# Kernel tuning notes

Measured on AMD Instinct MI355X. Metric: run time of the kernel, lower is better.

The kernel has to match this reference:

```python
import jax, jax.numpy as jnp
import numpy as np

N = 50000
E = 800000
IN = 3
H = 64
OUT = 128
L = 4


def _layernorm(x, w, b, eps=1e-5):
    mu = jnp.mean(x, axis=-1, keepdims=True)
    var = jnp.mean(jnp.square(x - mu), axis=-1, keepdims=True)
    return (x - mu) * jax.lax.rsqrt(var + eps) * w + b


def setup_inputs() -> dict:
    key = jax.random.key(0)
    ks = jax.random.split(key, 12)

    def lin(k, fan_in, shape):
        return jax.random.normal(k, shape, dtype=jnp.float32) / np.sqrt(fan_in)

    x = jax.random.normal(ks[0], (N, IN), dtype=jnp.float32)
    edge_index = jax.random.randint(ks[1], (2, E), 0, N, dtype=jnp.int32)
    return {
        "x": x,
        "edge_index": edge_index,
        "in_w": lin(ks[2], IN, (IN, H)), "in_b": jnp.zeros((H,), jnp.float32),
        "ew1": lin(ks[3], 2, (2, H)), "eb1": jnp.zeros((H,), jnp.float32),
        "ew2": lin(ks[4], H, (H, H)), "eb2": jnp.zeros((H,), jnp.float32),
        "cw1": lin(ks[5], H, (L, H, H)), "cb1": jnp.zeros((L, H), jnp.float32),
        "cw2": lin(ks[6], H, (L, H, H)), "cb2": jnp.zeros((L, H), jnp.float32),
        "lnw": jnp.ones((L, H), jnp.float32), "lnb": jnp.zeros((L, H), jnp.float32),
        "fw": lin(ks[7], H, (H, OUT)), "fb": jnp.zeros((OUT,), jnp.float32),
        "rw": lin(ks[8], H, (H, OUT)), "rb": jnp.zeros((OUT,), jnp.float32),
        "ow": jnp.ones((OUT,), jnp.float32), "ob": jnp.zeros((OUT,), jnp.float32),
    }


def reference(x, edge_index, in_w, in_b, ew1, eb1, ew2, eb2,
              cw1, cb1, cw2, cb2, lnw, lnb, fw, fb, rw, rb, ow, ob):
    pos = x[:, :2]
    row, col = edge_index[0], edge_index[1]  # source, target (PyG convention)
    rel_pos = pos[col] - pos[row]                              # [E, 2]
    edge_attr = jnp.maximum(rel_pos @ ew1 + eb1, 0.0) @ ew2 + eb2  # [E, H]

    h = x @ in_w + in_b  # [N, H]
    for i in range(L):
        identity = h
        # GINEConv (eps=0): mlp(x_i + sum_j relu(x_j + e_ij))
        msg = jax.nn.relu(h[row] + edge_attr)                  # [E, H]
        agg = jax.ops.segment_sum(msg, col, num_segments=N)    # [N, H]
        m = h + agg
        m = jnp.maximum(m @ cw1[i] + cb1[i], 0.0) @ cw2[i] + cb2[i]
        m = _layernorm(m, lnw[i], lnb[i])
        h = jax.nn.gelu(m, approximate=False) + identity

    out = (h @ fw + fb) + (h @ rw + rb)
    return _layernorm(out, ow, ob)
```

## Files before the change

### kernel.cpp

```cpp
#include <hip/hip_runtime.h>
#include <hip/hip_fp16.h>
#include <stdint.h>

#define NN 50000
#define NE 800000
#define SCAN_BLOCKS 196

typedef _Float16 half8v __attribute__((ext_vector_type(8)));
typedef float f32x4 __attribute__((ext_vector_type(4)));

static __device__ __forceinline__ __half2 u2h2(unsigned int u) {
    union { unsigned int u; __half2 h; } c; c.u = u; return c.h;
}
static __device__ __forceinline__ unsigned int h22u(__half2 h) {
    union { __half2 h; unsigned int u; } c; c.h = h; return c.u;
}

static __device__ __forceinline__ float4 fma4(float4 a, float s, float4 w) {
    a.x = fmaf(s, w.x, a.x); a.y = fmaf(s, w.y, a.y);
    a.z = fmaf(s, w.z, a.z); a.w = fmaf(s, w.w, a.w);
    return a;
}
static __device__ __forceinline__ void acch(float4& acc, uint2 h, uint2 e) {
    float2 h0 = __half22float2(u2h2(h.x));
    float2 h1 = __half22float2(u2h2(h.y));
    float2 e0 = __half22float2(u2h2(e.x));
    float2 e1 = __half22float2(u2h2(e.y));
    acc.x += fmaxf(h0.x + e0.x, 0.f);
    acc.y += fmaxf(h0.y + e0.y, 0.f);
    acc.z += fmaxf(h1.x + e1.x, 0.f);
    acc.w += fmaxf(h1.y + e1.y, 0.f);
}

__global__ __launch_bounds__(256) void k_deg(const int* __restrict__ ei, int* __restrict__ offcur) {
    int e = blockIdx.x * 256 + threadIdx.x;
    atomicAdd(&offcur[ei[NE + e]], 1);
}

__global__ __launch_bounds__(256) void k_scanA(const int* __restrict__ off, int* __restrict__ part) {
    __shared__ int s[256];
    int t = threadIdx.x;
    int idx = blockIdx.x * 256 + t;
    int d = (idx < NN) ? off[idx] : 0;
    s[t] = d; __syncthreads();
    for (int o = 128; o > 0; o >>= 1) {
        if (t < o) s[t] += s[t + o];
        __syncthreads();
    }
    if (t == 0) part[blockIdx.x] = s[0];
}

__global__ __launch_bounds__(256) void k_scanB(int* __restrict__ part) {
    __shared__ int s[256];
    int t = threadIdx.x;
    int d = (t < SCAN_BLOCKS) ? part[t] : 0;
    s[t] = d; __syncthreads();
    #pragma unroll
    for (int o = 1; o < 256; o <<= 1) {
        int v = (t >= o) ? s[t - o] : 0;
        __syncthreads();
        s[t] += v;
        __syncthreads();
    }
    if (t < SCAN_BLOCKS) part[t] = s[t] - d;
}

__global__ __launch_bounds__(256) void k_scanC(int* __restrict__ off, const int* __restrict__ part) {
    __shared__ int s[256];
    int t = threadIdx.x;
    int idx = blockIdx.x * 256 + t;
    int d = (idx < NN) ? off[idx] : 0;
    s[t] = d; __syncthreads();
    #pragma unroll
    for (int o = 1; o < 256; o <<= 1) {
        int v = (t >= o) ? s[t - o] : 0;
        __syncthreads();
        s[t] += v;
        __syncthreads();
    }
    if (idx < NN) off[idx] = s[t] - d + part[blockIdx.x];
}

__global__ __launch_bounds__(256) void k_scatter(const int* __restrict__ ei,
        int* __restrict__ offcur, unsigned short* __restrict__ rows, int* __restrict__ dpos) {
    int e = blockIdx.x * 256 + threadIdx.x;
    int col = ei[NE + e];
    int pos = atomicAdd(&offcur[col], 1);
    rows[pos] = (unsigned short)ei[e];
    dpos[e] = pos;
}

__global__ __launch_bounds__(256) void k_prep(const float* __restrict__ ew2, __half* __restrict__ w2f) {
    int tid = threadIdx.x;
    for (int i = tid; i < 4096; i += 256) {
        int k = i >> 6, n = i & 63;
        int kt = k >> 5, kin = k & 31;
        int quad = kin >> 3, j = kin & 7;
        int nt = n >> 4, nin = n & 15;
        w2f[(size_t)((kt * 4 + nt) * 64 + quad * 16 + nin) * 8 + j] = __float2half(ew2[i]);
    }
}

__global__ __launch_bounds__(256) void k_input(const float* __restrict__ x,
        const float* __restrict__ in_w, const float* __restrict__ in_b,
        __half* __restrict__ Ah) {
    int n = blockIdx.x * 4 + (threadIdx.x >> 6);
    int k = threadIdx.x & 63;
    const float* xr = x + (size_t)n * 3;
    float v = in_b[k] + xr[0] * in_w[k] + xr[1] * in_w[64 + k] + xr[2] * in_w[128 + k];
    Ah[(size_t)n * 64 + k] = __float2half(v);
}

__global__ __launch_bounds__(256) void k_edge(const float* __restrict__ x,
        const int* __restrict__ ei,
        const float* __restrict__ ew1, const float* __restrict__ eb1,
        const float* __restrict__ eb2, const __half* __restrict__ w2f,
        const int* __restrict__ dpos, __half* __restrict__ ea) {
    __shared__ float s_w1[128], s_b1[64], s_b2[64];
    __shared__ float s_rx[256], s_ry[256];
    __shared__ int s_pos[256];
    __shared__ __half s_d[4][16][80];
    int tid = threadIdx.x, lane = tid & 63, w = tid >> 6;

    half8v bf[8];
    {
        const half8v* W2F = (const half8v*)w2f;
        #pragma unroll
        for (int f = 0; f < 8; ++f) bf[f] = W2F[f * 64 + lane];
    }
    if (tid < 128) s_w1[tid] = ew1[tid];
    if (tid < 64) s_b1[tid] = eb1[tid];
    else if (tid < 128) s_b2[tid - 64] = eb2[tid - 64];
    int eb = blockIdx.x * 256;
    {
        int e = eb + tid;
        int r = ei[e], c = ei[NE + e];
        s_rx[tid] = x[(size_t)c * 3]     - x[(size_t)r * 3];
        s_ry[tid] = x[(size_t)c * 3 + 1] - x[(size_t)r * 3 + 1];
        s_pos[tid] = dpos[e];
    }
    __syncthreads();

    int lm = lane & 15, lq = lane >> 4;
    #pragma unroll
    for (int t = 0; t < 4; ++t) {
        int ebase = w * 64 + t * 16;
        float rx = s_rx[ebase + lm], ry = s_ry[ebase + lm];
        half8v a0, a1;
        #pragma unroll
        for (int j = 0; j < 8; ++j) {
            int k0 = lq * 8 + j;
            a0[j] = (_Float16)fmaxf(fmaf(rx, s_w1[k0], fmaf(ry, s_w1[64 + k0], s_b1[k0])), 0.f);
            int k1 = k0 + 32;
            a1[j] = (_Float16)fmaxf(fmaf(rx, s_w1[k1], fmaf(ry, s_w1[64 + k1], s_b1[k1])), 0.f);
        }
        f32x4 acc[4];
        #pragma unroll
        for (int nt = 0; nt < 4; ++nt) {
            float b = s_b2[nt * 16 + lm];
            acc[nt][0] = b; acc[nt][1] = b; acc[nt][2] = b; acc[nt][3] = b;
            acc[nt] = __builtin_amdgcn_mfma_f32_16x16x32_f16(a0, bf[nt],     acc[nt], 0, 0, 0);
            acc[nt] = __builtin_amdgcn_mfma_f32_16x16x32_f16(a1, bf[4 + nt], acc[nt], 0, 0, 0);
        }
        __builtin_amdgcn_wave_barrier();
        #pragma unroll
        for (int nt = 0; nt < 4; ++nt)
            #pragma unroll
            for (int r = 0; r < 4; ++r)
                s_d[w][lq * 4 + r][nt * 16 + lm] = __float2half(acc[nt][r]);
        __builtin_amdgcn_wave_barrier();
        int row = lane >> 2, seg = lane & 3;
        int pos = s_pos[w * 64 + t * 16 + row];
        uint4 v0 = *(const uint4*)&s_d[w][row][seg * 16];
        uint4 v1 = *(const uint4*)&s_d[w][row][seg * 16 + 8];
        uint4* dst = (uint4*)&ea[(size_t)pos * 64 + seg * 16];
        dst[0] = v0;
        dst[1] = v1;
        __builtin_amdgcn_wave_barrier();
    }
}

__global__ __launch_bounds__(256) void k_agg(const __half* __restrict__ Ah,
        const __half* __restrict__ ea, const unsigned short* __restrict__ rows,
        const int* __restrict__ offcur, float* __restrict__ M) {
    const uint2* A2 = (const uint2*)Ah;
    const uint2* E2 = (const uint2*)ea;
    int w = threadIdx.x >> 6, lane = threadIdx.x & 63;
    int es = lane >> 4, ch = lane & 15;
    int n = blockIdx.x * 4 + w;
    int p0 = (n == 0) ? 0 : offcur[n - 1];
    int p1 = offcur[n];
    float4 acc = {0,0,0,0}, accB = {0,0,0,0};
    for (int base = p0; base < p1; base += 64) {
        int cnt = min(64, p1 - base);
        int rl = (int)rows[base + min(lane, cnt - 1)];
        int j = 0;
        for (; j + 8 <= cnt; j += 8) {
            int i0 = j + es, i1 = j + 4 + es;
            int r0 = __shfl(rl, i0, 64);
            int r1 = __shfl(rl, i1, 64);
            uint2 h0 = A2[(size_t)r0 * 16 + ch];
            uint2 h1 = A2[(size_t)r1 * 16 + ch];
            uint2 e0 = E2[(size_t)(base + i0) * 16 + ch];
            uint2 e1 = E2[(size_t)(base + i1) * 16 + ch];
            acch(acc, h0, e0);
            acch(accB, h1, e1);
        }
        for (; j < cnt; j += 4) {
            int i0 = j + es;
            bool valid = i0 < cnt;
            int ic = valid ? i0 : (cnt - 1);
            int r0 = __shfl(rl, ic, 64);
            uint2 h0 = A2[(size_t)r0 * 16 + ch];
            uint2 e0 = E2[(size_t)(base + ic) * 16 + ch];
            if (valid) acch(acc, h0, e0);
        }
    }
    acc.x += accB.x; acc.y += accB.y; acc.z += accB.z; acc.w += accB.w;
    #pragma unroll
    for (int m = 16; m < 64; m <<= 1) {
        acc.x += __shfl_xor(acc.x, m, 64);
        acc.y += __shfl_xor(acc.y, m, 64);
        acc.z += __shfl_xor(acc.z, m, 64);
        acc.w += __shfl_xor(acc.w, m, 64);
    }
    if (es == 0) {
        uint2 su = A2[(size_t)n * 16 + ch];
        float2 s0 = __half22float2(u2h2(su.x));
        float2 s1 = __half22float2(u2h2(su.y));
        float4 o;
        o.x = s0.x + acc.x; o.y = s0.y + acc.y;
        o.z = s1.x + acc.z; o.w = s1.y + acc.w;
        *(float4*)&M[(size_t)n * 64 + ch * 4] = o;
    }
}

__global__ __launch_bounds__(256) void k_node(__half* __restrict__ Ah, const float* __restrict__ M,
        const float* __restrict__ cw1, const float* __restrict__ cb1,
        const float* __restrict__ cw2, const float* __restrict__ cb2,
        const float* __restrict__ lnw, const float* __restrict__ lnb) {
    __shared__ float s_W1[64 * 64];
    __shared__ float s_W2[64 * 64];
    __shared__ float s_m[64 * 68];
    __shared__ float s_b1[64], s_b2[64], s_g[64], s_bt[64];
    int tid = threadIdx.x;
    for (int i = tid; i < 4096; i += 256) { s_W1[i] = cw1[i]; s_W2[i] = cw2[i]; }
    if (tid < 64) { s_b1[tid] = cb1[tid]; s_g[tid] = lnw[tid]; }
    else if (tid < 128) { s_b2[tid - 64] = cb2[tid - 64]; s_bt[tid - 64] = lnb[tid - 64]; }
    int nb = blockIdx.x * 64;
    {
        const float4* M4 = (const float4*)(M + (size_t)nb * 64);
        #pragma unroll
        for (int q = 0; q < 4; ++q) {
            int i = q * 1024 + tid * 4;
            int nl = i >> 6, k = i & 63;
            float4 v = {0,0,0,0};
            if (nb + nl < NN) v = M4[i >> 2];
            *(float4*)&s_m[nl * 68 + k] = v;
        }
    }
    __syncthreads();

    int lane = tid & 63, w = tid >> 6;
    int cq = lane & 15, ng = lane >> 4;
    int rbase = w * 16 + ng * 4;
    int c0 = cq * 4;

    float4 acc[4];
    {
        float4 b1q = *(const float4*)&s_b1[c0];
        acc[0] = b1q; acc[1] = b1q; acc[2] = b1q; acc[3] = b1q;
    }
    #pragma unroll 4
    for (int k4 = 0; k4 < 16; ++k4) {
        float4 m0 = *(const float4*)&s_m[(rbase + 0) * 68 + k4 * 4];
        float4 m1 = *(const float4*)&s_m[(rbase + 1) * 68 + k4 * 4];
        float4 m2 = *(const float4*)&s_m[(rbase + 2) * 68 + k4 * 4];
        float4 m3 = *(const float4*)&s_m[(rbase + 3) * 68 + k4 * 4];
        #pragma unroll
        for (int kk = 0; kk < 4; ++kk) {
            float4 w4 = *(const float4*)&s_W1[(k4 * 4 + kk) * 64 + c0];
            acc[0] = fma4(acc[0], ((const float*)&m0)[kk], w4);
            acc[1] = fma4(acc[1], ((const float*)&m1)[kk], w4);
            acc[2] = fma4(acc[2], ((const float*)&m2)[kk], w4);
            acc[3] = fma4(acc[3], ((const float*)&m3)[kk], w4);
        }
    }
    __builtin_amdgcn_wave_barrier();
    #pragma unroll
    for (int j = 0; j < 4; ++j) {
        float4 u;
        u.x = fmaxf(acc[j].x, 0.f); u.y = fmaxf(acc[j].y, 0.f);
        u.z = fmaxf(acc[j].z, 0.f); u.w = fmaxf(acc[j].w, 0.f);
        *(float4*)&s_m[(rbase + j) * 68 + c0] = u;
    }
    __builtin_amdgcn_wave_barrier();

    {
        float4 b2q = *(const float4*)&s_b2[c0];
        acc[0] = b2q; acc[1] = b2q; acc[2] = b2q; acc[3] = b2q;
    }
    #pragma unroll 4
    for (int k4 = 0; k4 < 16; ++k4) {
        float4 m0 = *(const float4*)&s_m[(rbase + 0) * 68 + k4 * 4];
        float4 m1 = *(const float4*)&s_m[(rbase + 1) * 68 + k4 * 4];
        float4 m2 = *(const float4*)&s_m[(rbase + 2) * 68 + k4 * 4];
        float4 m3 = *(const float4*)&s_m[(rbase + 3) * 68 + k4 * 4];
        #pragma unroll
        for (int kk = 0; kk < 4; ++kk) {
            float4 w4 = *(const float4*)&s_W2[(k4 * 4 + kk) * 64 + c0];
            acc[0] = fma4(acc[0], ((const float*)&m0)[kk], w4);
            acc[1] = fma4(acc[1], ((const float*)&m1)[kk], w4);
            acc[2] = fma4(acc[2], ((const float*)&m2)[kk], w4);
            acc[3] = fma4(acc[3], ((const float*)&m3)[kk], w4);
        }
    }

    float4 gq  = *(const float4*)&s_g[c0];
    float4 btq = *(const float4*)&s_bt[c0];
    #pragma unroll
    for (int j = 0; j < 4; ++j) {
        float4 v = acc[j];
        float sum = v.x + v.y + v.z + v.w;
        float sq  = v.x * v.x + v.y * v.y + v.z * v.z + v.w * v.w;
        #pragma unroll
        for (int m = 1; m < 16; m <<= 1) {
            sum += __shfl_xor(sum, m, 64);
            sq  += __shfl_xor(sq, m, 64);
        }
        float mu  = sum * (1.f / 64.f);
        float var = sq * (1.f / 64.f) - mu * mu;
        float rs  = rsqrtf(var + 1e-5f);
        int n = nb + rbase + j;
        if (n < NN) {
            uint2 iu = *(const uint2*)&Ah[(size_t)n * 64 + c0];
            float2 i0 = __half22float2(u2h2(iu.x));
            float2 i1 = __half22float2(u2h2(iu.y));
            float4 o;
            float y;
            y = (v.x - mu) * rs * gq.x + btq.x; o.x = 0.5f * y * (1.f + erff(y * 0.70710678118654752f)) + i0.x;
            y = (v.y - mu) * rs * gq.y + btq.y; o.y = 0.5f * y * (1.f + erff(y * 0.70710678118654752f)) + i0.y;
            y = (v.z - mu) * rs * gq.z + btq.z; o.z = 0.5f * y * (1.f + erff(y * 0.70710678118654752f)) + i1.x;
            y = (v.w - mu) * rs * gq.w + btq.w; o.w = 0.5f * y * (1.f + erff(y * 0.70710678118654752f)) + i1.y;
            uint2 ou;
            ou.x = h22u(__floats2half2_rn(o.x, o.y));
            ou.y = h22u(__floats2half2_rn(o.z, o.w));
            *(uint2*)&Ah[(size_t)n * 64 + c0] = ou;
        }
    }
}

__global__ __launch_bounds__(256) void k_final(const __half* __restrict__ Ah,
        const float* __restrict__ fw, const float* __restrict__ fb,
        const float* __restrict__ rw, const float* __restrict__ rb,
        const float* __restrict__ ow, const float* __restrict__ ob,
        float* __restrict__ out) {
    __shared__ float s_W[64 * 128];
    __shared__ float s_h[32 * 68];
    __shared__ float s_b[128];
    __shared__ float s_red[32][4];
    int tid = threadIdx.x;
    for (int i = tid; i < 8192; i += 256) s_W[i] = fw[i] + rw[i];
    if (tid < 128) s_b[tid] = fb[tid] + rb[tid];
    int nb = blockIdx.x * 32;
    for (int i = tid; i < 2048; i += 256) {
        int nl = i >> 6, k = i & 63;
        int n = nb + nl;
        s_h[nl * 68 + k] = (n < NN) ? __half2float(Ah[(size_t)n * 64 + k]) : 0.f;
    }
    __syncthreads();

    int lane = tid & 63, w = tid >> 6;
    int chh = w & 1, nh = w >> 1;
    int cq = lane & 15, ng = lane >> 4;
    int c0 = chh * 64 + cq * 4;
    int rbase = nh * 16 + ng * 4;

    float4 acc[4];
    {
        float4 bq = *(const float4*)&s_b[c0];
        acc[0] = bq; acc[1] = bq; acc[2] = bq; acc[3] = bq;
    }
    #pragma unroll 4
    for (int k4 = 0; k4 < 16; ++k4) {
        float4 m0 = *(const float4*)&s_h[(rbase + 0) * 68 + k4 * 4];
        float4 m1 = *(const float4*)&s_h[(rbase + 1) * 68 + k4 * 4];
        float4 m2 = *(const float4*)&s_h[(rbase + 2) * 68 + k4 * 4];
        float4 m3 = *(const float4*)&s_h[(rbase + 3) * 68 + k4 * 4];
        #pragma unroll
        for (int kk = 0; kk < 4; ++kk) {
            float4 w4 = *(const float4*)&s_W[(k4 * 4 + kk) * 128 + c0];
            acc[0] = fma4(acc[0], ((const float*)&m0)[kk], w4);
            acc[1] = fma4(acc[1], ((const float*)&m1)[kk], w4);
            acc[2] = fma4(acc[2], ((const float*)&m2)[kk], w4);
            acc[3] = fma4(acc[3], ((const float*)&m3)[kk], w4);
        }
    }
    #pragma unroll
    for (int j = 0; j < 4; ++j) {
        float4 v = acc[j];
        float sum = v.x + v.y + v.z + v.w;
        float sq  = v.x * v.x + v.y * v.y + v.z * v.z + v.w * v.w;
        #pragma unroll
        for (int m = 1; m < 16; m <<= 1) {
            sum += __shfl_xor(sum, m, 64);
            sq  += __shfl_xor(sq, m, 64);
        }
        if (cq == 0) {
            s_red[rbase + j][chh * 2]     = sum;
            s_red[rbase + j][chh * 2 + 1] = sq;
        }
    }
    __syncthreads();
    float4 gq = *(const float4*)&ow[c0];
    float4 bq = *(const float4*)&ob[c0];
    #pragma unroll
    for (int j = 0; j < 4; ++j) {
        int nl = rbase + j;
        int n = nb + nl;
        float tsum = s_red[nl][0] + s_red[nl][2];
        float tsq  = s_red[nl][1] + s_red[nl][3];
        float mu  = tsum * (1.f / 128.f);
        float var = tsq * (1.f / 128.f) - mu * mu;
        float rs  = rsqrtf(var + 1e-5f);
        if (n < NN) {
            float4 v = acc[j];
            float4 o;
            o.x = (v.x - mu) * rs * gq.x + bq.x;
            o.y = (v.y - mu) * rs * gq.y + bq.y;
            o.z = (v.z - mu) * rs * gq.z + bq.z;
            o.w = (v.w - mu) * rs * gq.w + bq.w;
            *(float4*)&out[(size_t)n * 128 + c0] = o;
        }
    }
}

extern "C" void kernel_launch(void* const* d_in, const int* in_sizes, int n_in,
                              void* d_out, int out_size, void* d_ws, size_t ws_size,
                              hipStream_t stream) {
    const float* x    = (const float*)d_in[0];
    const int*   ei   = (const int*)d_in[1];
    const float* in_w = (const float*)d_in[2];
    const float* in_b = (const float*)d_in[3];
    const float* ew1  = (const float*)d_in[4];
    const float* eb1  = (const float*)d_in[5];
    const float* ew2  = (const float*)d_in[6];
    const float* eb2  = (const float*)d_in[7];
    const float* cw1  = (const float*)d_in[8];
    const float* cb1  = (const float*)d_in[9];
    const float* cw2  = (const float*)d_in[10];
    const float* cb2  = (const float*)d_in[11];
    const float* lnw  = (const float*)d_in[12];
    const float* lnb  = (const float*)d_in[13];
    const float* fw   = (const float*)d_in[14];
    const float* fb   = (const float*)d_in[15];
    const float* rw   = (const float*)d_in[16];
    const float* rb   = (const float*)d_in[17];
    const float* ow   = (const float*)d_in[18];
    const float* ob   = (const float*)d_in[19];
    float* out = (float*)d_out;

    char* ws = (char*)d_ws;
    __half*         ea   = (__half*)ws;
    __half*         Ah   = (__half*)(ws + 102400000);
    unsigned short* rows = (unsigned short*)(ws + 108800000);
    int*            off  = (int*)(ws + 110400000);
    float*          M    = (float*)(ws + 110600016);
    int*            dpos = (int*)M;
    int*            part = (int*)((char*)M + 3200000);
    __half*         w2f  = (__half*)((char*)M + 3300000);

    (void)hipMemsetAsync(off, 0, (NN + 1) * sizeof(int), stream);
    k_deg<<<NE / 256, 256, 0, stream>>>(ei, off);
    k_scanA<<<SCAN_BLOCKS, 256, 0, stream>>>(off, part);
    k_scanB<<<1, 256, 0, stream>>>(part);
    k_scanC<<<SCAN_BLOCKS, 256, 0, stream>>>(off, part);
    k_scatter<<<NE / 256, 256, 0, stream>>>(ei, off, rows, dpos);
    k_prep<<<1, 256, 0, stream>>>(ew2, w2f);
    k_input<<<NN / 4, 256, 0, stream>>>(x, in_w, in_b, Ah);
    k_edge<<<NE / 256, 256, 0, stream>>>(x, ei, ew1, eb1, eb2, w2f, dpos, ea);

    const int nodeBlocks = (NN + 63) / 64;
    for (int l = 0; l < 4; ++l) {
        k_agg<<<NN / 4, 256, 0, stream>>>(Ah, ea, rows, off, M);
        k_node<<<nodeBlocks, 256, 0, stream>>>(Ah, M,
            cw1 + (size_t)l * 4096, cb1 + (size_t)l * 64,
            cw2 + (size_t)l * 4096, cb2 + (size_t)l * 64,
            lnw + (size_t)l * 64,   lnb + (size_t)l * 64);
    }
    k_final<<<(NN + 31) / 32, 256, 0, stream>>>(Ah, fw, fb, rw, rb, ow, ob, out);
}
```

Measured before the change: 507.8 us.

## Fuse CSR scatter into edge kernel, widen agg loads, store M as fp16

Removes the separate k_scatter kernel by doing the atomic slot allocation and row write inside k_edge, which also drops the dpos buffer round trip. k_agg now loads 16-byte vectors (8 halfs per lane, 8 lanes per row) and handles 16 edges per iteration instead of 8. The aggregated M buffer is stored in fp16 rather than fp32, halving its write and read traffic between k_agg and k_node. The cost is an extra rounding of h+agg to half precision and atomics moved into the edge kernel.

```diff
diff --git a/kernel.cpp b/kernel.cpp
--- a/kernel.cpp
+++ b/kernel.cpp
@@ -21,15 +21,16 @@
     a.z = fmaf(s, w.z, a.z); a.w = fmaf(s, w.w, a.w);
     return a;
 }
-static __device__ __forceinline__ void acch(float4& acc, uint2 h, uint2 e) {
-    float2 h0 = __half22float2(u2h2(h.x));
-    float2 h1 = __half22float2(u2h2(h.y));
-    float2 e0 = __half22float2(u2h2(e.x));
-    float2 e1 = __half22float2(u2h2(e.y));
-    acc.x += fmaxf(h0.x + e0.x, 0.f);
-    acc.y += fmaxf(h0.y + e0.y, 0.f);
-    acc.z += fmaxf(h1.x + e1.x, 0.f);
-    acc.w += fmaxf(h1.y + e1.y, 0.f);
+static __device__ __forceinline__ void acc8(float* acc, float4 hv, float4 ev) {
+    const unsigned int* hu = (const unsigned int*)&hv;
+    const unsigned int* eu = (const unsigned int*)&ev;
+    #pragma unroll
+    for (int q = 0; q < 4; ++q) {
+        float2 hf = __half22float2(u2h2(hu[q]));
+        float2 ef = __half22float2(u2h2(eu[q]));
+        acc[q * 2]     += fmaxf(hf.x + ef.x, 0.f);
+        acc[q * 2 + 1] += fmaxf(hf.y + ef.y, 0.f);
+    }
 }
 
 __global__ __launch_bounds__(256) void k_deg(const int* __restrict__ ei, int* __restrict__ offcur) {
@@ -81,15 +82,6 @@
     if (idx < NN) off[idx] = s[t] - d + part[blockIdx.x];
 }
 
-__global__ __launch_bounds__(256) void k_scatter(const int* __restrict__ ei,
-        int* __restrict__ offcur, unsigned short* __restrict__ rows, int* __restrict__ dpos) {
-    int e = blockIdx.x * 256 + threadIdx.x;
-    int col = ei[NE + e];
-    int pos = atomicAdd(&offcur[col], 1);
-    rows[pos] = (unsigned short)ei[e];
-    dpos[e] = pos;
-}
-
 __global__ __launch_bounds__(256) void k_prep(const float* __restrict__ ew2, __half* __restrict__ w2f) {
     int tid = threadIdx.x;
     for (int i = tid; i < 4096; i += 256) {
@@ -115,7 +107,8 @@
         const int* __restrict__ ei,
         const float* __restrict__ ew1, const float* __restrict__ eb1,
         const float* __restrict__ eb2, const __half* __restrict__ w2f,
-        const int* __restrict__ dpos, __half* __restrict__ ea) {
+        int* __restrict__ offcur, unsigned short* __restrict__ rows,
+        __half* __restrict__ ea) {
     __shared__ float s_w1[128], s_b1[64], s_b2[64];
     __shared__ float s_rx[256], s_ry[256];
     __shared__ int s_pos[256];
@@ -137,7 +130,9 @@
         int r = ei[e], c = ei[NE + e];
         s_rx[tid] = x[(size_t)c * 3]     - x[(size_t)r * 3];
         s_ry[tid] = x[(size_t)c * 3 + 1] - x[(size_t)r * 3 + 1];
-        s_pos[tid] = dpos[e];
+        int pos = atomicAdd(&offcur[c], 1);
+        rows[pos] = (unsigned short)r;
+        s_pos[tid] = pos;
     }
     __syncthreads();
 
@@ -182,60 +177,62 @@
 
 __global__ __launch_bounds__(256) void k_agg(const __half* __restrict__ Ah,
         const __half* __restrict__ ea, const unsigned short* __restrict__ rows,
-        const int* __restrict__ offcur, float* __restrict__ M) {
-    const uint2* A2 = (const uint2*)Ah;
-    const uint2* E2 = (const uint2*)ea;
+        const int* __restrict__ offcur, __half* __restrict__ M) {
+    const float4* A4 = (const float4*)Ah;
+    const float4* E4 = (const float4*)ea;
     int w = threadIdx.x >> 6, lane = threadIdx.x & 63;
-    int es = lane >> 4, ch = lane & 15;
+    int es = lane >> 3, oc = lane & 7;
     int n = blockIdx.x * 4 + w;
     int p0 = (n == 0) ? 0 : offcur[n - 1];
     int p1 = offcur[n];
-    float4 acc = {0,0,0,0}, accB = {0,0,0,0};
+    float acc[8] = {0,0,0,0,0,0,0,0};
+    float accB[8] = {0,0,0,0,0,0,0,0};
     for (int base = p0; base < p1; base += 64) {
         int cnt = min(64, p1 - base);
         int rl = (int)rows[base + min(lane, cnt - 1)];
         int j = 0;
-        for (; j + 8 <= cnt; j += 8) {
-            int i0 = j + es, i1 = j + 4 + es;
+        for (; j + 16 <= cnt; j += 16) {
+            int i0 = j + es, i1 = j + 8 + es;
             int r0 = __shfl(rl, i0, 64);
             int r1 = __shfl(rl, i1, 64);
-            uint2 h0 = A2[(size_t)r0 * 16 + ch];
-            uint2 h1 = A2[(size_t)r1 * 16 + ch];
-            uint2 e0 = E2[(size_t)(base + i0) * 16 + ch];
-            uint2 e1 = E2[(size_t)(base + i1) * 16 + ch];
-            acch(acc, h0, e0);
-            acch(accB, h1, e1);
-        }
-        for (; j < cnt; j += 4) {
+            float4 h0 = A4[(size_t)r0 * 8 + oc];
+            float4 h1 = A4[(size_t)r1 * 8 + oc];
+            float4 e0 = E4[(size_t)(base + i0) * 8 + oc];
+            float4 e1 = E4[(size_t)(base + i1) * 8 + oc];
+            acc8(acc, h0, e0);
+            acc8(accB, h1, e1);
+        }
+        for (; j < cnt; j += 8) {
             int i0 = j + es;
             bool valid = i0 < cnt;
             int ic = valid ? i0 : (cnt - 1);
             int r0 = __shfl(rl, ic, 64);
-            uint2 h0 = A2[(size_t)r0 * 16 + ch];
-            uint2 e0 = E2[(size_t)(base + ic) * 16 + ch];
-            if (valid) acch(acc, h0, e0);
-        }
-    }
-    acc.x += accB.x; acc.y += accB.y; acc.z += accB.z; acc.w += accB.w;
-    #pragma unroll
-    for (int m = 16; m < 64; m <<= 1) {
-        acc.x += __shfl_xor(acc.x, m, 64);
-        acc.y += __shfl_xor(acc.y, m, 64);
-        acc.z += __shfl_xor(acc.z, m, 64);
-        acc.w += __shfl_xor(acc.w, m, 64);
+            float4 h0 = A4[(size_t)r0 * 8 + oc];
+            float4 e0 = E4[(size_t)(base + ic) * 8 + oc];
+            if (valid) acc8(acc, h0, e0);
+        }
+    }
+    #pragma unroll
+    for (int q = 0; q < 8; ++q) acc[q] += accB[q];
+    #pragma unroll
+    for (int m = 8; m < 64; m <<= 1) {
+        #pragma unroll
+        for (int q = 0; q < 8; ++q) acc[q] += __shfl_xor(acc[q], m, 64);
     }
     if (es == 0) {
-        uint2 su = A2[(size_t)n * 16 + ch];
-        float2 s0 = __half22float2(u2h2(su.x));
-        float2 s1 = __half22float2(u2h2(su.y));
-        float4 o;
-        o.x = s0.x + acc.x; o.y = s0.y + acc.y;
-        o.z = s1.x + acc.z; o.w = s1.y + acc.w;
-        *(float4*)&M[(size_t)n * 64 + ch * 4] = o;
-    }
-}
-
-__global__ __launch_bounds__(256) void k_node(__half* __restrict__ Ah, const float* __restrict__ M,
+        float4 sv = A4[(size_t)n * 8 + oc];
+        const unsigned int* su = (const unsigned int*)&sv;
+        unsigned int o[4];
+        #pragma unroll
+        for (int q = 0; q < 4; ++q) {
+            float2 sf = __half22float2(u2h2(su[q]));
+            o[q] = h22u(__floats2half2_rn(sf.x + acc[q * 2], sf.y + acc[q * 2 + 1]));
+        }
+        *(uint4*)&M[(size_t)n * 64 + oc * 8] = *(uint4*)&o[0];
+    }
+}
+
+__global__ __launch_bounds__(256) void k_node(__half* __restrict__ Ah, const __half* __restrict__ M,
         const float* __restrict__ cw1, const float* __restrict__ cb1,
         const float* __restrict__ cw2, const float* __restrict__ cb2,
         const float* __restrict__ lnw, const float* __restrict__ lnb) {
@@ -249,14 +246,21 @@
     else if (tid < 128) { s_b2[tid - 64] = cb2[tid - 64]; s_bt[tid - 64] = lnb[tid - 64]; }
     int nb = blockIdx.x * 64;
     {
-        const float4* M4 = (const float4*)(M + (size_t)nb * 64);
-        #pragma unroll
-        for (int q = 0; q < 4; ++q) {
-            int i = q * 1024 + tid * 4;
-            int nl = i >> 6, k = i & 63;
-            float4 v = {0,0,0,0};
-            if (nb + nl < NN) v = M4[i >> 2];
-            *(float4*)&s_m[nl * 68 + k] = v;
+        const uint4* M4 = (const uint4*)(M + (size_t)nb * 64);
+        #pragma unroll
+        for (int q = 0; q < 2; ++q) {
+            int i = q * 256 + tid;
+            int nl = i >> 3;
+            int k8 = (i & 7) * 8;
+            uint4 v = {0, 0, 0, 0};
+            if (nb + nl < NN) v = M4[i];
+            float* dst = &s_m[nl * 68 + k8];
+            const unsigned int* vu = (const unsigned int*)&v;
+            #pragma unroll
+            for (int p = 0; p < 4; ++p) {
+                float2 f = __half22float2(u2h2(vu[p]));
+                dst[p * 2] = f.x; dst[p * 2 + 1] = f.y;
+            }
         }
     }
     __syncthreads();
@@ -465,20 +469,18 @@
     __half*         Ah   = (__half*)(ws + 102400000);
     unsigned short* rows = (unsigned short*)(ws + 108800000);
     int*            off  = (int*)(ws + 110400000);
-    float*          M    = (float*)(ws + 110600016);
-    int*            dpos = (int*)M;
-    int*            part = (int*)((char*)M + 3200000);
-    __half*         w2f  = (__half*)((char*)M + 3300000);
+    __half*         M    = (__half*)(ws + 110600016);
+    int*            part = (int*)M;
+    __half*         w2f  = (__half*)((char*)M + 100000);
 
     (void)hipMemsetAsync(off, 0, (NN + 1) * sizeof(int), stream);
     k_deg<<<NE / 256, 256, 0, stream>>>(ei, off);
     k_scanA<<<SCAN_BLOCKS, 256, 0, stream>>>(off, part);
     k_scanB<<<1, 256, 0, stream>>>(part);
     k_scanC<<<SCAN_BLOCKS, 256, 0, stream>>>(off, part);
-    k_scatter<<<NE / 256, 256, 0, stream>>>(ei, off, rows, dpos);
     k_prep<<<1, 256, 0, stream>>>(ew2, w2f);
     k_input<<<NN / 4, 256, 0, stream>>>(x, in_w, in_b, Ah);
-    k_edge<<<NE / 256, 256, 0, stream>>>(x, ei, ew1, eb1, eb2, w2f, dpos, ea);
+    k_edge<<<NE / 256, 256, 0, stream>>>(x, ei, ew1, eb1, eb2, w2f, off, rows, ea);
 
     const int nodeBlocks = (NN + 63) / 64;
     for (int l = 0; l < 4; ++l) {
```

Result: faster. 477.4 us (-6.0%).
